# Performance work log

Measured on AMD Instinct MI355X. Metric: run time of the kernel, lower is better.

## Reference

```python
import jax, jax.numpy as jnp
import numpy as np

ALPHA = 0.05
KSIZE = 7
SIGMA = 7.0  # SecondMomentMatrixLayer calls get_gaussian_kernel(ksize, ksize)


def _gaussian_kernel(ksize, sigma):
    ax = np.arange(ksize, dtype=np.float32) - (ksize - 1) / 2.0
    g1 = np.exp(-(ax ** 2) / (2.0 * sigma ** 2))
    g2 = np.outer(g1, g1)
    g2 = g2 / g2.sum()
    return jnp.asarray(g2, dtype=jnp.float32)


def setup_inputs() -> dict:
    key = jax.random.key(0)
    x = jax.random.uniform(key, (1, 1, 2048, 4096), dtype=jnp.float32)
    # Sobel filters (cross-correlation weights, as torch conv2d uses)
    wx = jnp.array([[-1., 0., 1.], [-2., 0., 2.], [-1., 0., 1.]], dtype=jnp.float32)
    wy = wx.T
    sobel_w = jnp.stack([wx, wy], axis=0)[:, None]  # (2,1,3,3)
    gauss_w = _gaussian_kernel(KSIZE, SIGMA)[None, None]  # (1,1,7,7)
    return {"x": x, "sobel_w": sobel_w, "gauss_w": gauss_w}


def _conv_same(x, w, groups=1):
    # x: (N,C,H,W), w: (O,C/g,kh,kw); torch-style cross-correlation, SAME padding
    return jax.lax.conv_general_dilated(
        x, w, window_strides=(1, 1), padding="SAME",
        dimension_numbers=("NCHW", "OIHW", "NCHW"),
        feature_group_count=groups)


def reference(x, sobel_w, gauss_w):
    # 1) image gradients: (N,1,H,W) -> (N,2,H,W)
    g = _conv_same(x, sobel_w)
    ix, iy = g[:, 0], g[:, 1]  # (N,H,W)
    # 2) channel products Ixx, Iyy, Ixy: (N,3,H,W)
    prod = jnp.stack([ix * ix, iy * iy, ix * iy], axis=1)
    # 3) Gaussian smoothing of each channel (same kernel depthwise)
    gw3 = jnp.broadcast_to(gauss_w, (3, 1, KSIZE, KSIZE))
    s = _conv_same(prod, gw3, groups=3)
    sxx, syy, sxy = s[:, 0], s[:, 1], s[:, 2]  # (N,H,W)
    # 4) corner response R = det - alpha*trace^2 (with the original's extra unsqueeze(0))
    r = (sxx * syy - sxy * sxy) - ALPHA * ((sxx + syy) ** 2)[None]  # (1,N,H,W) -> (1,1,H,W) for N=1
    # 5) NMS: threshold at (lower) median, 7x7 stride-1 maxpool, equality mask, multiply
    flat = r.ravel()
    k = (flat.shape[0] - 1) // 2  # torch.median -> lower median
    med = jnp.partition(flat, k)[k]
    thr = jnp.where(r > med, r, jnp.float32(0))
    pooled = jax.lax.reduce_window(
        thr, -jnp.inf, jax.lax.max, (1, 1, KSIZE, KSIZE), (1, 1, 1, 1), "SAME")
    mask = jnp.where(pooled == thr, jnp.float32(1), jnp.float32(0))
    return mask * r
```

## Files before the change

kernel.cpp:

```cpp
#include <hip/hip_runtime.h>
#include <hip/hip_bf16.h>
#include <math.h>

#define H 2048
#define W 4096
#define NPIX (H * W)
#define KSEL 4194303u
#define NT 512
#define TSX 64
#define TSY 32
#define NBX (W / TSX)
#define NBY (H / TSY)

__device__ __forceinline__ unsigned fmap(float f) {
    unsigned u = __float_as_uint(f);
    return (u & 0x80000000u) ? ~u : (u | 0x80000000u);
}
__device__ __forceinline__ float4 ld4s(const float* p) { return *(const float4*)p; }
__device__ __forceinline__ void st4s(float* p, float4 v) { *(float4*)p = v; }
__device__ __forceinline__ void ld12(const float* p, float* d) {
    float4 a = ld4s(p), b = ld4s(p + 4), c = ld4s(p + 8);
    d[0]=a.x; d[1]=a.y; d[2]=a.z; d[3]=a.w;
    d[4]=b.x; d[5]=b.y; d[6]=b.z; d[7]=b.w;
    d[8]=c.x; d[9]=c.y; d[10]=c.z; d[11]=c.w;
}
__device__ __forceinline__ unsigned aload(const unsigned* p) {
    return __hip_atomic_load(p, __ATOMIC_RELAXED, __HIP_MEMORY_SCOPE_AGENT);
}

#define SMF 13224
#define SXA(r,c) smem[5472 + (r)*76 + (c)]
#define GXA(r,c) smem[(r)*72 + (c)]
#define GYA(r,c) smem[2736 + (r)*72 + (c)]
#define H0A(r,c) smem[5472 + (r)*68 + (c)]
#define H1A(r,c) smem[8056 + (r)*68 + (c)]
#define H2A(r,c) smem[10640 + (r)*68 + (c)]

__global__ __launch_bounds__(NT) void k_response(const float* __restrict__ x,
                                                 const float* __restrict__ gw,
                                                 float* __restrict__ r,
                                                 unsigned* __restrict__ hist1) {
    __shared__ float smem[SMF];
    unsigned* lh = (unsigned*)smem;

    int tl = threadIdx.x;
    int bx = blockIdx.x & (NBX - 1);
    int by = blockIdx.x >> 6;
    int tx0 = bx * TSX, ty0 = by * TSY;
    bool interior = ((unsigned)(bx - 1) < 62u) && ((unsigned)(by - 1) < 62u);

    float hwr[7], vwr[7];
    float g33 = gw[24];
#pragma unroll
    for (int b = 0; b < 7; ++b) hwr[b] = gw[21 + b];
#pragma unroll
    for (int a = 0; a < 7; ++a) vwr[a] = gw[a * 7 + 3] / g33;

#pragma unroll
    for (int it = 0; it < 2; ++it) {
        int task = tl + it * NT;
        if (task < 720) {
            int row = task / 18, g = task - row * 18;
            int gy = ty0 - 4 + row;
            int gx0 = tx0 - 4 + 4 * g;
            float4 v;
            if (interior) {
                v = *(const float4*)&x[(size_t)gy * W + gx0];
            } else {
                v = make_float4(0.f, 0.f, 0.f, 0.f);
                if ((unsigned)gy < H) {
                    if ((unsigned)gx0 <= (unsigned)(W - 4)) {
                        v = *(const float4*)&x[(size_t)gy * W + gx0];
                    } else {
                        float* vv = (float*)&v;
#pragma unroll
                        for (int k = 0; k < 4; ++k) {
                            int c = gx0 + k;
                            if ((unsigned)c < W) vv[k] = x[(size_t)gy * W + c];
                        }
                    }
                }
            }
            st4s(&SXA(row, 4 * g), v);
        }
    }
    __syncthreads();

#pragma unroll
    for (int it = 0; it < 2; ++it) {
        int task = tl + it * NT;
        if (task < 684) {
            int row = task / 18, g = task - row * 18;
            int base = 4 * g;
            float w0[8], w1[8], w2[8];
            {
                float4 t0 = ld4s(&SXA(row, base)), t1 = ld4s(&SXA(row, base + 4));
                w0[0]=t0.x; w0[1]=t0.y; w0[2]=t0.z; w0[3]=t0.w; w0[4]=t1.x; w0[5]=t1.y; w0[6]=t1.z; w0[7]=t1.w;
                t0 = ld4s(&SXA(row + 1, base)); t1 = ld4s(&SXA(row + 1, base + 4));
                w1[0]=t0.x; w1[1]=t0.y; w1[2]=t0.z; w1[3]=t0.w; w1[4]=t1.x; w1[5]=t1.y; w1[6]=t1.z; w1[7]=t1.w;
                t0 = ld4s(&SXA(row + 2, base)); t1 = ld4s(&SXA(row + 2, base + 4));
                w2[0]=t0.x; w2[1]=t0.y; w2[2]=t0.z; w2[3]=t0.w; w2[4]=t1.x; w2[5]=t1.y; w2[6]=t1.z; w2[7]=t1.w;
            }
            float4 gxv, gyv;
            float* pgx = (float*)&gxv;
            float* pgy = (float*)&gyv;
            if (interior) {
#pragma unroll
                for (int k = 0; k < 4; ++k) {
                    pgx[k] = (w0[k + 2] - w0[k]) + 2.f * (w1[k + 2] - w1[k]) + (w2[k + 2] - w2[k]);
                    pgy[k] = (w2[k] - w0[k]) + 2.f * (w2[k + 1] - w0[k + 1]) + (w2[k + 2] - w0[k + 2]);
                }
            } else {
                int rowOK = ((unsigned)(ty0 - 3 + row) < H);
#pragma unroll
                for (int k = 0; k < 4; ++k) {
                    float ixv = (w0[k + 2] - w0[k]) + 2.f * (w1[k + 2] - w1[k]) + (w2[k + 2] - w2[k]);
                    float iyv = (w2[k] - w0[k]) + 2.f * (w2[k + 1] - w0[k + 1]) + (w2[k + 2] - w0[k + 2]);
                    int gc = tx0 + base + k - 3;
                    bool ok = rowOK && ((unsigned)gc < W);
                    pgx[k] = ok ? ixv : 0.f;
                    pgy[k] = ok ? iyv : 0.f;
                }
            }
            st4s(&GXA(row, base), gxv);
            st4s(&GYA(row, base), gyv);
        }
    }
    __syncthreads();

#pragma unroll
    for (int it = 0; it < 2; ++it) {
        int task = tl + it * NT;
        if (task < 608) {
            int row = task >> 4, c0 = (task & 15) * 4;
            float wgx[12], wgy[12];
            ld12(&GXA(row, c0), wgx);
            ld12(&GYA(row, c0), wgy);
            float px[10], py[10], pxy[10];
#pragma unroll
            for (int i = 0; i < 10; ++i) {
                px[i] = wgx[i] * wgx[i];
                py[i] = wgy[i] * wgy[i];
                pxy[i] = wgx[i] * wgy[i];
            }
            float4 s0, s1, s2;
            float* q0 = (float*)&s0; float* q1 = (float*)&s1; float* q2 = (float*)&s2;
#pragma unroll
            for (int k = 0; k < 4; ++k) {
                float a0 = 0.f, a1 = 0.f, a2 = 0.f;
#pragma unroll
                for (int b = 0; b < 7; ++b) {
                    float w = hwr[b];
                    a0 += w * px[k + b];
                    a1 += w * py[k + b];
                    a2 += w * pxy[k + b];
                }
                q0[k] = a0; q1[k] = a1; q2[k] = a2;
            }
            st4s(&H0A(row, c0), s0);
            st4s(&H1A(row, c0), s1);
            st4s(&H2A(row, c0), s2);
        }
    }
    __syncthreads();

    if (tl < 256) lh[tl] = 0;
    __syncthreads();

    {
        int ii = tl >> 4, c0 = (tl & 15) * 4;
        float4 a0 = make_float4(0.f, 0.f, 0.f, 0.f), a1 = a0, a2 = a0;
#pragma unroll
        for (int a = 0; a < 7; ++a) {
            float w = vwr[a];
            float4 h0v = ld4s(&H0A(ii + a, c0));
            float4 h1v = ld4s(&H1A(ii + a, c0));
            float4 h2v = ld4s(&H2A(ii + a, c0));
            a0.x += w * h0v.x; a0.y += w * h0v.y; a0.z += w * h0v.z; a0.w += w * h0v.w;
            a1.x += w * h1v.x; a1.y += w * h1v.y; a1.z += w * h1v.z; a1.w += w * h1v.w;
            a2.x += w * h2v.x; a2.y += w * h2v.y; a2.z += w * h2v.z; a2.w += w * h2v.w;
        }
        float* sxx = (float*)&a0; float* syy = (float*)&a1; float* sxy = (float*)&a2;
        float4 rv4;
        float* prv = (float*)&rv4;
#pragma unroll
        for (int k = 0; k < 4; ++k) {
            float tr = sxx[k] + syy[k];
            prv[k] = sxx[k] * syy[k] - sxy[k] * sxy[k] - 0.05f * tr * tr;
        }
        st4s(&r[(size_t)(ty0 + ii) * W + tx0 + c0], rv4);
#pragma unroll
        for (int k = 0; k < 4; ++k) atomicAdd(&lh[fmap(prv[k]) >> 24], 1u);
    }
    __syncthreads();
    if (tl < 256 && lh[tl]) atomicAdd(&hist1[tl], lh[tl]);
}

__global__ __launch_bounds__(256) void k_scan256(const unsigned* __restrict__ hist,
                                                 unsigned* __restrict__ sel,
                                                 int in_rank_idx, int out_base) {
    __shared__ unsigned s[256];
    int t = threadIdx.x;
    unsigned c = hist[t];
    s[t] = c;
    __syncthreads();
    for (int off = 1; off < 256; off <<= 1) {
        unsigned v = (t >= off) ? s[t - off] : 0u;
        __syncthreads();
        s[t] += v;
        __syncthreads();
    }
    unsigned k = (in_rank_idx < 0) ? KSEL : sel[in_rank_idx];
    unsigned cumb = s[t] - c;
    if (k >= cumb && k < s[t]) {
        sel[out_base] = (unsigned)t;
        sel[out_base + 1] = k - cumb;
    }
}

__global__ __launch_bounds__(256) void k_hist2(const float* __restrict__ r,
                                               unsigned* __restrict__ sel,
                                               unsigned* __restrict__ hist2,
                                               unsigned* __restrict__ tick) {
    __shared__ unsigned lh[256];
    __shared__ unsigned lastf;
    int t = threadIdx.x;
    lh[t] = 0;
    __syncthreads();
    unsigned b1 = sel[0];
    int idx = blockIdx.x * blockDim.x + t;
    int stride = gridDim.x * blockDim.x;
    const float4* r4 = (const float4*)r;
    for (int i = idx; i < NPIX / 4; i += stride) {
        float4 v = r4[i];
        unsigned u;
        u = fmap(v.x); if ((u >> 24) == b1) atomicAdd(&lh[(u >> 16) & 0xFF], 1u);
        u = fmap(v.y); if ((u >> 24) == b1) atomicAdd(&lh[(u >> 16) & 0xFF], 1u);
        u = fmap(v.z); if ((u >> 24) == b1) atomicAdd(&lh[(u >> 16) & 0xFF], 1u);
        u = fmap(v.w); if ((u >> 24) == b1) atomicAdd(&lh[(u >> 16) & 0xFF], 1u);
    }
    __syncthreads();
    if (lh[t]) atomicAdd(&hist2[t], lh[t]);
    __syncthreads();

    if (t == 0)
        lastf = (__hip_atomic_fetch_add(tick, 1u, __ATOMIC_ACQ_REL, __HIP_MEMORY_SCOPE_AGENT)
                 == (unsigned)(gridDim.x - 1)) ? 1u : 0u;
    __syncthreads();
    if (lastf) {
        unsigned c = aload(&hist2[t]);
        lh[t] = c;
        __syncthreads();
        for (int off = 1; off < 256; off <<= 1) {
            unsigned v = (t >= off) ? lh[t - off] : 0u;
            __syncthreads();
            lh[t] += v;
            __syncthreads();
        }
        unsigned k = sel[1];
        unsigned cumb = lh[t] - c;
        if (k >= cumb && k < lh[t]) { sel[2] = (unsigned)t; sel[3] = k - cumb; }
    }
}

__global__ __launch_bounds__(256) void k_hist3(const float* __restrict__ r,
                                               const unsigned* __restrict__ sel,
                                               unsigned* __restrict__ hist3) {
    unsigned top16 = (sel[0] << 8) | sel[2];
    int idx = blockIdx.x * blockDim.x + threadIdx.x;
    int stride = gridDim.x * blockDim.x;
    const float4* r4 = (const float4*)r;
    for (int i = idx; i < NPIX / 4; i += stride) {
        float4 v = r4[i];
        unsigned u;
        u = fmap(v.x); if ((u >> 16) == top16) atomicAdd(&hist3[u & 0xFFFF], 1u);
        u = fmap(v.y); if ((u >> 16) == top16) atomicAdd(&hist3[u & 0xFFFF], 1u);
        u = fmap(v.z); if ((u >> 16) == top16) atomicAdd(&hist3[u & 0xFFFF], 1u);
        u = fmap(v.w); if ((u >> 16) == top16) atomicAdd(&hist3[u & 0xFFFF], 1u);
    }
}

__global__ __launch_bounds__(1024) void k_scan64k(const unsigned* __restrict__ hist3,
                                                  unsigned* __restrict__ sel) {
    __shared__ unsigned ps[1024];
    int t = threadIdx.x;
    const uint4* h4 = (const uint4*)hist3;
    unsigned sum = 0;
#pragma unroll
    for (int i = 0; i < 16; ++i) {
        uint4 v = h4[t * 16 + i];
        sum += v.x + v.y + v.z + v.w;
    }
    ps[t] = sum;
    __syncthreads();
    for (int off = 1; off < 1024; off <<= 1) {
        unsigned v = (t >= off) ? ps[t - off] : 0u;
        __syncthreads();
        ps[t] += v;
        __syncthreads();
    }
    unsigned k = sel[3];
    unsigned inc = ps[t], cumb = inc - sum;
    if (k >= cumb && k < inc) {
        unsigned rem = k - cumb;
        unsigned cum = 0, b3 = 0;
        for (int i = 0; i < 64; ++i) {
            unsigned c = hist3[t * 64 + i];
            if (rem < cum + c) { b3 = (unsigned)(t * 64 + i); break; }
            cum += c;
        }
        unsigned med_u = (sel[0] << 24) | (sel[2] << 16) | b3;
        unsigned bits = (med_u & 0x80000000u) ? (med_u & 0x7FFFFFFFu) : ~med_u;
        ((float*)sel)[6] = __uint_as_float(bits);
    }
}

#define RT(r,c) smem[(r)*72 + (c)]
#define HM(r,c) smem[2736 + (r)*64 + (c)]

__global__ __launch_bounds__(NT) void k_final(const float* __restrict__ r,
                                              const unsigned* __restrict__ sel,
                                              float* __restrict__ out) {
    __shared__ float smem[5168];
    float med = ((const float*)sel)[6];
    int tl = threadIdx.x;
    int bx = blockIdx.x & (NBX - 1);
    int by = blockIdx.x >> 6;
    int tx0 = bx * TSX, ty0 = by * TSY;
    bool interior = ((unsigned)(bx - 1) < 62u) && ((unsigned)(by - 1) < 62u);
    const float NINF = -INFINITY;

#pragma unroll
    for (int it = 0; it < 2; ++it) {
        int task = tl + it * NT;
        if (task < 684) {
            int row = task / 18, g = task - row * 18;
            int gy = ty0 - 3 + row;
            int gx0 = tx0 - 4 + 4 * g;
            float4 v;
            if (interior) {
                v = *(const float4*)&r[(size_t)gy * W + gx0];
            } else {
                v = make_float4(NINF, NINF, NINF, NINF);
                if ((unsigned)gy < H) {
                    if ((unsigned)gx0 <= (unsigned)(W - 4)) {
                        v = *(const float4*)&r[(size_t)gy * W + gx0];
                    } else {
                        float* pv = (float*)&v;
#pragma unroll
                        for (int k = 0; k < 4; ++k) {
                            int c = gx0 + k;
                            if ((unsigned)c < W) pv[k] = r[(size_t)gy * W + c];
                        }
                    }
                }
            }
            st4s(&RT(row, 4 * g), v);
        }
    }
    __syncthreads();

#pragma unroll
    for (int it = 0; it < 2; ++it) {
        int task = tl + it * NT;
        if (task < 608) {
            int row = task >> 4, c0 = (task & 15) << 2;
            float w[12];
            ld12(&RT(row, c0), w);
            float th[11];
#pragma unroll
            for (int j = 1; j <= 10; ++j) {
                float v = w[j];
                th[j] = (v > med) ? v : ((v == NINF) ? NINF : 0.f);
            }
            float4 m4;
            float* pm = (float*)&m4;
#pragma unroll
            for (int k = 0; k < 4; ++k) {
                float m = th[k + 1];
#pragma unroll
                for (int b = 2; b < 8; ++b) m = fmaxf(m, th[k + b]);
                pm[k] = m;
            }
            st4s(&HM(row, c0), m4);
        }
    }
    __syncthreads();

    {
        int ii = tl >> 4, c0 = (tl & 15) << 2;
        float4 m = ld4s(&HM(ii, c0));
#pragma unroll
        for (int a = 1; a < 7; ++a) {
            float4 h = ld4s(&HM(ii + a, c0));
            m.x = fmaxf(m.x, h.x); m.y = fmaxf(m.y, h.y);
            m.z = fmaxf(m.z, h.z); m.w = fmaxf(m.w, h.w);
        }
        float4 rv = ld4s(&RT(ii + 3, c0 + 4));
        float4 o;
        float tvx = (rv.x > med) ? rv.x : 0.f;
        float tvy = (rv.y > med) ? rv.y : 0.f;
        float tvz = (rv.z > med) ? rv.z : 0.f;
        float tvw = (rv.w > med) ? rv.w : 0.f;
        o.x = (m.x == tvx) ? rv.x : 0.f;
        o.y = (m.y == tvy) ? rv.y : 0.f;
        o.z = (m.z == tvz) ? rv.z : 0.f;
        o.w = (m.w == tvw) ? rv.w : 0.f;
        st4s(&out[(size_t)(ty0 + ii) * W + tx0 + c0], o);
    }
}

extern "C" void kernel_launch(void* const* d_in, const int* in_sizes, int n_in,
                              void* d_out, int out_size, void* d_ws, size_t ws_size,
                              hipStream_t stream) {
    const float* x = (const float*)d_in[0];
    const float* gw = (const float*)d_in[2];
    float* out = (float*)d_out;

    char* ws = (char*)d_ws;
    float* r = (float*)ws;
    unsigned* base = (unsigned*)(ws + (size_t)NPIX * 4);
    unsigned* hist1 = base;
    unsigned* hist2 = base + 256;
    unsigned* hist3 = base + 512;
    unsigned* sel   = base + 66048;
    unsigned* tick  = base + 66064;

    hipMemsetAsync(base, 0, 66068u * sizeof(unsigned), stream);

    int nblk = NBX * NBY;
    k_response<<<nblk, NT, 0, stream>>>(x, gw, r, hist1);
    k_scan256<<<1, 256, 0, stream>>>(hist1, sel, -1, 0);
    k_hist2<<<1024, 256, 0, stream>>>(r, sel, hist2, tick);
    k_hist3<<<1024, 256, 0, stream>>>(r, sel, hist3);
    k_scan64k<<<1, 1024, 0, stream>>>(hist3, sel);
    k_final<<<nblk, NT, 0, stream>>>(r, sel, out);
}
```

Before: 146.9 us.

## Fuse first histogram scan into response kernel, use direct-to-LDS loads, dedupe atomics

Removes the separate k_scan256 launch: the last block of k_response, found with an atomic ticket counter, scans the coarse histogram and writes the selected bucket. Interior tiles load the input halo straight into LDS with global_load_lds, which needs the SXA row stride changed from 76 to 72 so rows are packed contiguously. The per-thread LDS histogram update now merges duplicate bins among each thread's four values before issuing atomics. This adds a grid-wide atomic and a serial tail in one block, and relies on the packed layout matching the wave-wide LDS write pattern of the builtin.

```diff
diff --git a/kernel.cpp b/kernel.cpp
--- a/kernel.cpp
+++ b/kernel.cpp
@@ -27,9 +27,15 @@
 __device__ __forceinline__ unsigned aload(const unsigned* p) {
     return __hip_atomic_load(p, __ATOMIC_RELAXED, __HIP_MEMORY_SCOPE_AGENT);
 }
+__device__ __forceinline__ void gload16(const float* g, float* l) {
+    __builtin_amdgcn_global_load_lds(
+        (const __attribute__((address_space(1))) unsigned int*)g,
+        (__attribute__((address_space(3))) unsigned int*)l,
+        16, 0, 0);
+}
 
 #define SMF 13224
-#define SXA(r,c) smem[5472 + (r)*76 + (c)]
+#define SXA(r,c) smem[5472 + (r)*72 + (c)]
 #define GXA(r,c) smem[(r)*72 + (c)]
 #define GYA(r,c) smem[2736 + (r)*72 + (c)]
 #define H0A(r,c) smem[5472 + (r)*68 + (c)]
@@ -39,8 +45,11 @@
 __global__ __launch_bounds__(NT) void k_response(const float* __restrict__ x,
                                                  const float* __restrict__ gw,
                                                  float* __restrict__ r,
-                                                 unsigned* __restrict__ hist1) {
+                                                 unsigned* __restrict__ hist1,
+                                                 unsigned* __restrict__ sel,
+                                                 unsigned* __restrict__ tick) {
     __shared__ float smem[SMF];
+    __shared__ unsigned lastf;
     unsigned* lh = (unsigned*)smem;
 
     int tl = threadIdx.x;
@@ -56,18 +65,27 @@
 #pragma unroll
     for (int a = 0; a < 7; ++a) vwr[a] = gw[a * 7 + 3] / g33;
 
-#pragma unroll
-    for (int it = 0; it < 2; ++it) {
-        int task = tl + it * NT;
-        if (task < 720) {
-            int row = task / 18, g = task - row * 18;
-            int gy = ty0 - 4 + row;
-            int gx0 = tx0 - 4 + 4 * g;
-            float4 v;
-            if (interior) {
-                v = *(const float4*)&x[(size_t)gy * W + gx0];
-            } else {
-                v = make_float4(0.f, 0.f, 0.f, 0.f);
+    if (interior) {
+#pragma unroll
+        for (int it = 0; it < 2; ++it) {
+            int task = tl + it * NT;
+            if (task < 720) {
+                int row = task / 18, g = task - row * 18;
+                int gy = ty0 - 4 + row;
+                int gx0 = tx0 - 4 + 4 * g;
+                int base_task = (tl & ~63) + it * NT;
+                gload16(&x[(size_t)gy * W + gx0], &smem[5472 + base_task * 4]);
+            }
+        }
+    } else {
+#pragma unroll
+        for (int it = 0; it < 2; ++it) {
+            int task = tl + it * NT;
+            if (task < 720) {
+                int row = task / 18, g = task - row * 18;
+                int gy = ty0 - 4 + row;
+                int gx0 = tx0 - 4 + 4 * g;
+                float4 v = make_float4(0.f, 0.f, 0.f, 0.f);
                 if ((unsigned)gy < H) {
                     if ((unsigned)gx0 <= (unsigned)(W - 4)) {
                         v = *(const float4*)&x[(size_t)gy * W + gx0];
@@ -80,8 +98,8 @@
                         }
                     }
                 }
-            }
-            st4s(&SXA(row, 4 * g), v);
+                st4s(&SXA(row, 4 * g), v);
+            }
         }
     }
     __syncthreads();
@@ -189,32 +207,45 @@
             prv[k] = sxx[k] * syy[k] - sxy[k] * sxy[k] - 0.05f * tr * tr;
         }
         st4s(&r[(size_t)(ty0 + ii) * W + tx0 + c0], rv4);
-#pragma unroll
-        for (int k = 0; k < 4; ++k) atomicAdd(&lh[fmap(prv[k]) >> 24], 1u);
+        unsigned bn[4];
+#pragma unroll
+        for (int k = 0; k < 4; ++k) bn[k] = fmap(prv[k]) >> 24;
+#pragma unroll
+        for (int i = 0; i < 4; ++i) {
+            bool dup = false;
+            unsigned cnt = 1;
+#pragma unroll
+            for (int j = 0; j < 4; ++j) {
+                if (j < i) dup = dup || (bn[j] == bn[i]);
+                if (j > i) cnt += (bn[j] == bn[i]) ? 1u : 0u;
+            }
+            if (!dup) atomicAdd(&lh[bn[i]], cnt);
+        }
     }
     __syncthreads();
     if (tl < 256 && lh[tl]) atomicAdd(&hist1[tl], lh[tl]);
-}
-
-__global__ __launch_bounds__(256) void k_scan256(const unsigned* __restrict__ hist,
-                                                 unsigned* __restrict__ sel,
-                                                 int in_rank_idx, int out_base) {
-    __shared__ unsigned s[256];
-    int t = threadIdx.x;
-    unsigned c = hist[t];
-    s[t] = c;
-    __syncthreads();
-    for (int off = 1; off < 256; off <<= 1) {
-        unsigned v = (t >= off) ? s[t - off] : 0u;
+    __syncthreads();
+
+    if (tl == 0)
+        lastf = (__hip_atomic_fetch_add(tick, 1u, __ATOMIC_ACQ_REL, __HIP_MEMORY_SCOPE_AGENT)
+                 == (unsigned)(gridDim.x - 1)) ? 1u : 0u;
+    __syncthreads();
+    if (lastf) {
+        unsigned* ss = (unsigned*)smem + 256;
+        unsigned c = 0;
+        if (tl < 256) { c = aload(&hist1[tl]); ss[tl] = c; }
         __syncthreads();
-        s[t] += v;
-        __syncthreads();
-    }
-    unsigned k = (in_rank_idx < 0) ? KSEL : sel[in_rank_idx];
-    unsigned cumb = s[t] - c;
-    if (k >= cumb && k < s[t]) {
-        sel[out_base] = (unsigned)t;
-        sel[out_base + 1] = k - cumb;
+        for (int off = 1; off < 256; off <<= 1) {
+            unsigned v = 0;
+            if (tl >= off && tl < 256) v = ss[tl - off];
+            __syncthreads();
+            if (tl < 256) ss[tl] += v;
+            __syncthreads();
+        }
+        if (tl < 256) {
+            unsigned inc = ss[tl], cumb = inc - c;
+            if (KSEL >= cumb && KSEL < inc) { sel[0] = (unsigned)tl; sel[1] = KSEL - cumb; }
+        }
     }
 }
 
@@ -429,9 +460,8 @@
     hipMemsetAsync(base, 0, 66068u * sizeof(unsigned), stream);
 
     int nblk = NBX * NBY;
-    k_response<<<nblk, NT, 0, stream>>>(x, gw, r, hist1);
-    k_scan256<<<1, 256, 0, stream>>>(hist1, sel, -1, 0);
-    k_hist2<<<1024, 256, 0, stream>>>(r, sel, hist2, tick);
+    k_response<<<nblk, NT, 0, stream>>>(x, gw, r, hist1, sel, tick);
+    k_hist2<<<1024, 256, 0, stream>>>(r, sel, hist2, tick + 1);
     k_hist3<<<1024, 256, 0, stream>>>(r, sel, hist3);
     k_scan64k<<<1, 1024, 0, stream>>>(hist3, sel);
     k_final<<<nblk, NT, 0, stream>>>(r, sel, out);
```

Result: slower. 229.5 us (+56.2%).
